# Kernel optimization log

Hardware: AMD Instinct MI355X
Metric: run time of the kernel (lower is better)

## Reference

```python
import jax, jax.numpy as jnp
import numpy as np

N = 50000      # nodes
E = 800000     # edges
XS = 64        # x_size
ES = 32        # edge_attr dim (in_size = XS + ES = 96)
OUT = 64       # out_size
H = 128        # hidden_size
EPS = 1e-5


def _lin_init(k, fan_in, fan_out):
    s = 1.0 / np.sqrt(fan_in)
    kw, kb = jax.random.split(k)
    w = jax.random.uniform(kw, (fan_in, fan_out), minval=-s, maxval=s, dtype=jnp.float32)
    b = jax.random.uniform(kb, (fan_out,), minval=-s, maxval=s, dtype=jnp.float32)
    return w, b


def setup_inputs() -> dict:
    key = jax.random.key(0)
    ks = jax.random.split(key, 12)
    x = jax.random.normal(ks[0], (N, XS), dtype=jnp.float32)
    edge_index = jax.random.randint(ks[1], (2, E), 0, N, dtype=jnp.int64)
    edge_attr = jax.random.normal(ks[2], (E, ES), dtype=jnp.float32)
    u = jax.random.normal(ks[3], (1, 8), dtype=jnp.float32)
    batch = jnp.zeros((N,), dtype=jnp.int64)
    # MLP1: (96->128) LReLU (128->128) LReLU (128->64) LReLU LN(64)
    m1w0, m1b0 = _lin_init(ks[4], XS + ES, H)
    m1w1, m1b1 = _lin_init(ks[5], H, H)
    m1w2, m1b2 = _lin_init(ks[6], H, OUT)
    ln1_g = jnp.ones((OUT,), jnp.float32); ln1_b = jnp.zeros((OUT,), jnp.float32)
    # MLP2: (128->128) LReLU (128->128) LReLU (128->64) LReLU LN(64)
    m2w0, m2b0 = _lin_init(ks[7], XS + OUT, H)
    m2w1, m2b1 = _lin_init(ks[8], H, H)
    m2w2, m2b2 = _lin_init(ks[9], H, OUT)
    ln2_g = jnp.ones((OUT,), jnp.float32); ln2_b = jnp.zeros((OUT,), jnp.float32)
    return dict(x=x, edge_index=edge_index, edge_attr=edge_attr, u=u, batch=batch,
                m1w0=m1w0, m1b0=m1b0, m1w1=m1w1, m1b1=m1b1, m1w2=m1w2, m1b2=m1b2,
                ln1_g=ln1_g, ln1_b=ln1_b,
                m2w0=m2w0, m2b0=m2b0, m2w1=m2w1, m2b1=m2b1, m2w2=m2w2, m2b2=m2b2,
                ln2_g=ln2_g, ln2_b=ln2_b)


def _lrelu(v):
    return jax.nn.leaky_relu(v, 0.01)


def _layernorm(v, g, b):
    mu = jnp.mean(v, axis=-1, keepdims=True)
    var = jnp.mean(jnp.square(v - mu), axis=-1, keepdims=True)
    return (v - mu) * jax.lax.rsqrt(var + EPS) * g + b


def _mlp(h, w0, b0, w1, b1, w2, b2, g, bn):
    h = _lrelu(h @ w0 + b0)
    h = _lrelu(h @ w1 + b1)
    h = _lrelu(h @ w2 + b2)          # activate_last=True
    return _layernorm(h, g, bn)      # layer_norm=True


def reference(x, edge_index, edge_attr, u, batch,
              m1w0, m1b0, m1w1, m1b1, m1w2, m1b2, ln1_g, ln1_b,
              m2w0, m2b0, m2w1, m2b1, m2w2, m2b2, ln2_g, ln2_b):
    row, col = edge_index[0], edge_index[1]
    # gather source nodes, concat edge features -> per-edge MLP
    h = jnp.concatenate([x[row], edge_attr], axis=1)            # [E, 96]
    h = _mlp(h, m1w0, m1b0, m1w1, m1b1, m1w2, m1b2, ln1_g, ln1_b)  # [E, 64]
    # scatter_mean over destination nodes
    agg = jax.ops.segment_sum(h, col, num_segments=N)           # [N, 64]
    cnt = jax.ops.segment_sum(jnp.ones((E,), h.dtype), col, num_segments=N)
    agg = agg / jnp.maximum(cnt, 1.0)[:, None]
    # node update MLP
    h2 = jnp.concatenate([x, agg], axis=1)                      # [N, 128]
    return _mlp(h2, m2w0, m2b0, m2w1, m2b1, m2w2, m2b2, ln2_g, ln2_b)
```

## Files before the change

kernel.cpp:

```cpp
#include <hip/hip_runtime.h>


#define NNODES 50000
#define NEDGES 800000

typedef __bf16 bf16;
typedef __bf16 __attribute__((ext_vector_type(4))) bf16x4;
typedef __bf16 __attribute__((ext_vector_type(8))) bf16x8;
typedef float __attribute__((ext_vector_type(4))) f32x4;

__device__ __forceinline__ f32x4 mfma_bf16(bf16x8 a, bf16x8 b, f32x4 c) {
    return __builtin_amdgcn_mfma_f32_16x16x32_bf16(a, b, c, 0, 0, 0);
}


__global__ void prep_weights(const float* __restrict__ w10, const float* __restrict__ w11,
                             const float* __restrict__ w12, const float* __restrict__ w20,
                             const float* __restrict__ w21, const float* __restrict__ w22,
                             bf16* __restrict__ img) {
    int idx = blockIdx.x * 256 + threadIdx.x;
    float f;
    if (idx < 13312) {
        int n = idx / 104, k = idx % 104;
        f = (k < 96) ? w10[k * 128 + n] : 0.0f;
    } else if (idx < 30720) {
        int t = idx - 13312; int n = t / 136, k = t % 136;
        f = (k < 128) ? w11[k * 128 + n] : 0.0f;
    } else if (idx < 39424) {
        int t = idx - 30720; int n = t / 136, k = t % 136;
        f = (k < 128) ? w12[k * 64 + n] : 0.0f;
    } else if (idx < 56832) {
        int t = idx - 39424; int n = t / 136, k = t % 136;
        f = (k < 128) ? w20[k * 128 + n] : 0.0f;
    } else if (idx < 74240) {
        int t = idx - 56832; int n = t / 136, k = t % 136;
        f = (k < 128) ? w21[k * 128 + n] : 0.0f;
    } else if (idx < 82944) {
        int t = idx - 74240; int n = t / 136, k = t % 136;
        f = (k < 128) ? w22[k * 64 + n] : 0.0f;
    } else {
        return;
    }
    img[idx] = (bf16)f;
}

__global__ __launch_bounds__(256) void edge_mlp(
    const float* __restrict__ x, const int* __restrict__ eidx,
    const float* __restrict__ eattr, const bf16* __restrict__ wimg,
    const float* __restrict__ b0g, const float* __restrict__ b1g,
    const float* __restrict__ b2g, const float* __restrict__ lng,
    const float* __restrict__ lnb, float* __restrict__ agg, float* __restrict__ cnt) {
    __shared__ __align__(16) bf16 wall[39424];
    __shared__ __align__(16) bf16 atile[128 * 104];
    __shared__ __align__(16) bf16 hid[128 * 136];
    __shared__ float bs[448];

    const int tid = threadIdx.x;
    {
        const uint4* src = (const uint4*)wimg;
        uint4* dst = (uint4*)wall;
        for (int i = tid; i < 4928; i += 256) dst[i] = src[i];
    }
    if (tid < 128) { bs[tid] = b0g[tid]; bs[128 + tid] = b1g[tid]; }
    else {
        int t = tid - 128;
        if (t < 64) { bs[256 + t] = b2g[t]; bs[320 + t] = lng[t]; bs[384 + t] = lnb[t]; }
    }
    __syncthreads();

    const int lane = tid & 63;
    const int wv = tid >> 6;
    const int col16 = lane & 15;
    const int quad = lane >> 4;

    float b0r[8], b1r[8], b2r[4], gr[4], br[4];
#pragma unroll
    for (int i = 0; i < 8; i++) { b0r[i] = bs[i * 16 + col16]; b1r[i] = bs[128 + i * 16 + col16]; }
#pragma unroll
    for (int i = 0; i < 4; i++) {
        b2r[i] = bs[256 + i * 16 + col16];
        gr[i] = bs[320 + i * 16 + col16];
        br[i] = bs[384 + i * 16 + col16];
    }

    const bf16* w0t = wall;
    const bf16* w1t = wall + 13312;
    const bf16* w2t = wall + 30720;

    const int ebase = blockIdx.x * 128;
    const f32x4 vzero = {0.0f, 0.0f, 0.0f, 0.0f};

    {
        const int el = tid >> 1, half = tid & 1;
        const int e = ebase + el;
        const int r = eidx[e];
        const float4* xs = (const float4*)(x + (size_t)r * 64);
        bf16* arow = atile + el * 104;
#pragma unroll
        for (int j = 0; j < 8; j++) {
            float4 v = xs[half * 8 + j];
            bf16x4 u = {(bf16)v.x, (bf16)v.y, (bf16)v.z, (bf16)v.w};
            *(bf16x4*)(arow + half * 32 + j * 4) = u;
        }
        const float4* es = (const float4*)(eattr + (size_t)e * 32);
#pragma unroll
        for (int j = 0; j < 4; j++) {
            float4 v = es[half * 4 + j];
            bf16x4 u = {(bf16)v.x, (bf16)v.y, (bf16)v.z, (bf16)v.w};
            *(bf16x4*)(arow + 64 + half * 16 + j * 4) = u;
        }
    }

    const int r0 = wv * 32 + col16;
    const int rw = wv * 32 + quad * 4;

    f32x4 acc1[2][8];
#pragma unroll
    for (int mt = 0; mt < 2; mt++)
#pragma unroll
        for (int nt = 0; nt < 8; nt++) acc1[mt][nt] = vzero;
#pragma unroll
    for (int ks = 0; ks < 3; ks++) {
        bf16x8 a0 = *(const bf16x8*)(atile + r0 * 104 + ks * 32 + quad * 8);
        bf16x8 a1 = *(const bf16x8*)(atile + (r0 + 16) * 104 + ks * 32 + quad * 8);
#pragma unroll
        for (int nt = 0; nt < 8; nt++) {
            bf16x8 b = *(const bf16x8*)(w0t + (nt * 16 + col16) * 104 + ks * 32 + quad * 8);
            acc1[0][nt] = mfma_bf16(a0, b, acc1[0][nt]);
            acc1[1][nt] = mfma_bf16(a1, b, acc1[1][nt]);
        }
    }
#pragma unroll
    for (int mt = 0; mt < 2; mt++)
#pragma unroll
        for (int nt = 0; nt < 8; nt++)
#pragma unroll
            for (int rg = 0; rg < 4; rg++) {
                float v = acc1[mt][nt][rg] + b0r[nt];
                v = (v > 0.0f) ? v : 0.01f * v;
                hid[(rw + mt * 16 + rg) * 136 + nt * 16 + col16] = (bf16)v;
            }

    bf16x8 a2[2][4];
#pragma unroll
    for (int mt = 0; mt < 2; mt++)
#pragma unroll
        for (int ks = 0; ks < 4; ks++)
            a2[mt][ks] = *(const bf16x8*)(hid + (r0 + mt * 16) * 136 + ks * 32 + quad * 8);
    f32x4 acc2[2][8];
#pragma unroll
    for (int mt = 0; mt < 2; mt++)
#pragma unroll
        for (int nt = 0; nt < 8; nt++) acc2[mt][nt] = vzero;
#pragma unroll
    for (int ks = 0; ks < 4; ks++) {
#pragma unroll
        for (int nt = 0; nt < 8; nt++) {
            bf16x8 b = *(const bf16x8*)(w1t + (nt * 16 + col16) * 136 + ks * 32 + quad * 8);
            acc2[0][nt] = mfma_bf16(a2[0][ks], b, acc2[0][nt]);
            acc2[1][nt] = mfma_bf16(a2[1][ks], b, acc2[1][nt]);
        }
    }
#pragma unroll
    for (int mt = 0; mt < 2; mt++)
#pragma unroll
        for (int nt = 0; nt < 8; nt++)
#pragma unroll
            for (int rg = 0; rg < 4; rg++) {
                float v = acc2[mt][nt][rg] + b1r[nt];
                v = (v > 0.0f) ? v : 0.01f * v;
                hid[(rw + mt * 16 + rg) * 136 + nt * 16 + col16] = (bf16)v;
            }

    bf16x8 a3[2][4];
#pragma unroll
    for (int mt = 0; mt < 2; mt++)
#pragma unroll
        for (int ks = 0; ks < 4; ks++)
            a3[mt][ks] = *(const bf16x8*)(hid + (r0 + mt * 16) * 136 + ks * 32 + quad * 8);
    f32x4 acc3[2][4];
#pragma unroll
    for (int mt = 0; mt < 2; mt++)
#pragma unroll
        for (int nt = 0; nt < 4; nt++) acc3[mt][nt] = vzero;
#pragma unroll
    for (int ks = 0; ks < 4; ks++) {
#pragma unroll
        for (int nt = 0; nt < 4; nt++) {
            bf16x8 b = *(const bf16x8*)(w2t + (nt * 16 + col16) * 136 + ks * 32 + quad * 8);
            acc3[0][nt] = mfma_bf16(a3[0][ks], b, acc3[0][nt]);
            acc3[1][nt] = mfma_bf16(a3[1][ks], b, acc3[1][nt]);
        }
    }

    const int* cidx = eidx + NEDGES;
#pragma unroll
    for (int mt = 0; mt < 2; mt++) {
        float vals[4][4];
        float s1[4] = {0.f, 0.f, 0.f, 0.f}, s2[4] = {0.f, 0.f, 0.f, 0.f};
#pragma unroll
        for (int nt = 0; nt < 4; nt++)
#pragma unroll
            for (int rg = 0; rg < 4; rg++) {
                float v = acc3[mt][nt][rg] + b2r[nt];
                v = (v > 0.0f) ? v : 0.01f * v;
                vals[nt][rg] = v;
                s1[rg] += v;
                s2[rg] += v * v;
            }
#pragma unroll
        for (int off = 1; off < 16; off <<= 1) {
#pragma unroll
            for (int rg = 0; rg < 4; rg++) {
                s1[rg] += __shfl_xor(s1[rg], off);
                s2[rg] += __shfl_xor(s2[rg], off);
            }
        }
#pragma unroll
        for (int rg = 0; rg < 4; rg++) {
            float mu = s1[rg] * 0.015625f;
            float var = s2[rg] * 0.015625f - mu * mu;
            float rstd = rsqrtf(var + 1e-5f);
            int e = ebase + rw + mt * 16 + rg;
            int c = cidx[e];
            float* dst = agg + (size_t)c * 64;
#pragma unroll
            for (int nt = 0; nt < 4; nt++) {
                float o = (vals[nt][rg] - mu) * rstd * gr[nt] + br[nt];
                atomicAdd(dst + nt * 16 + col16, o);
            }
            if (col16 == 0) atomicAdd(cnt + c, 1.0f);
        }
    }
}

__global__ __launch_bounds__(256) void node_mlp(
    const float* __restrict__ x, const float* __restrict__ agg,
    const float* __restrict__ cnt, const bf16* __restrict__ wimg,
    const float* __restrict__ b0g, const float* __restrict__ b1g,
    const float* __restrict__ b2g, const float* __restrict__ lng,
    const float* __restrict__ lnb, float* __restrict__ out) {
    __shared__ __align__(16) bf16 wall[43520];
    __shared__ __align__(16) bf16 atile[128 * 136];
    __shared__ __align__(16) bf16 hid[128 * 136];
    __shared__ float bs[448];

    const int tid = threadIdx.x;
    {
        const uint4* src = (const uint4*)wimg;
        uint4* dst = (uint4*)wall;
        for (int i = tid; i < 5440; i += 256) dst[i] = src[i];
    }
    if (tid < 128) { bs[tid] = b0g[tid]; bs[128 + tid] = b1g[tid]; }
    else {
        int t = tid - 128;
        if (t < 64) { bs[256 + t] = b2g[t]; bs[320 + t] = lng[t]; bs[384 + t] = lnb[t]; }
    }
    __syncthreads();

    const int lane = tid & 63;
    const int wv = tid >> 6;
    const int col16 = lane & 15;
    const int quad = lane >> 4;

    float b0r[8], b1r[8], b2r[4], gr[4], br[4];
#pragma unroll
    for (int i = 0; i < 8; i++) { b0r[i] = bs[i * 16 + col16]; b1r[i] = bs[128 + i * 16 + col16]; }
#pragma unroll
    for (int i = 0; i < 4; i++) {
        b2r[i] = bs[256 + i * 16 + col16];
        gr[i] = bs[320 + i * 16 + col16];
        br[i] = bs[384 + i * 16 + col16];
    }

    const bf16* w0t = wall;
    const bf16* w1t = wall + 17408;
    const bf16* w2t = wall + 34816;

    const int nbase = blockIdx.x * 128;
    const f32x4 vzero = {0.0f, 0.0f, 0.0f, 0.0f};

    {
        const int el = tid >> 1, half = tid & 1;
        int i = nbase + el;
        if (i >= NNODES) i = NNODES - 1;
        const float4* xs = (const float4*)(x + (size_t)i * 64);
        bf16* arow = atile + el * 136;
#pragma unroll
        for (int j = 0; j < 8; j++) {
            float4 v = xs[half * 8 + j];
            bf16x4 u = {(bf16)v.x, (bf16)v.y, (bf16)v.z, (bf16)v.w};
            *(bf16x4*)(arow + half * 32 + j * 4) = u;
        }
        float inv = 1.0f / fmaxf(cnt[i], 1.0f);
        const float4* as = (const float4*)(agg + (size_t)i * 64);
#pragma unroll
        for (int j = 0; j < 8; j++) {
            float4 v = as[half * 8 + j];
            bf16x4 u = {(bf16)(v.x * inv), (bf16)(v.y * inv), (bf16)(v.z * inv), (bf16)(v.w * inv)};
            *(bf16x4*)(arow + 64 + half * 32 + j * 4) = u;
        }
    }

    const int r0 = wv * 32 + col16;
    const int rw = wv * 32 + quad * 4;

    f32x4 acc1[2][8];
#pragma unroll
    for (int mt = 0; mt < 2; mt++)
#pragma unroll
        for (int nt = 0; nt < 8; nt++) acc1[mt][nt] = vzero;
#pragma unroll
    for (int ks = 0; ks < 4; ks++) {
        bf16x8 a0 = *(const bf16x8*)(atile + r0 * 136 + ks * 32 + quad * 8);
        bf16x8 a1 = *(const bf16x8*)(atile + (r0 + 16) * 136 + ks * 32 + quad * 8);
#pragma unroll
        for (int nt = 0; nt < 8; nt++) {
            bf16x8 b = *(const bf16x8*)(w0t + (nt * 16 + col16) * 136 + ks * 32 + quad * 8);
            acc1[0][nt] = mfma_bf16(a0, b, acc1[0][nt]);
            acc1[1][nt] = mfma_bf16(a1, b, acc1[1][nt]);
        }
    }
#pragma unroll
    for (int mt = 0; mt < 2; mt++)
#pragma unroll
        for (int nt = 0; nt < 8; nt++)
#pragma unroll
            for (int rg = 0; rg < 4; rg++) {
                float v = acc1[mt][nt][rg] + b0r[nt];
                v = (v > 0.0f) ? v : 0.01f * v;
                hid[(rw + mt * 16 + rg) * 136 + nt * 16 + col16] = (bf16)v;
            }

    bf16x8 a2[2][4];
#pragma unroll
    for (int mt = 0; mt < 2; mt++)
#pragma unroll
        for (int ks = 0; ks < 4; ks++)
            a2[mt][ks] = *(const bf16x8*)(hid + (r0 + mt * 16) * 136 + ks * 32 + quad * 8);
    f32x4 acc2[2][8];
#pragma unroll
    for (int mt = 0; mt < 2; mt++)
#pragma unroll
        for (int nt = 0; nt < 8; nt++) acc2[mt][nt] = vzero;
#pragma unroll
    for (int ks = 0; ks < 4; ks++) {
#pragma unroll
        for (int nt = 0; nt < 8; nt++) {
            bf16x8 b = *(const bf16x8*)(w1t + (nt * 16 + col16) * 136 + ks * 32 + quad * 8);
            acc2[0][nt] = mfma_bf16(a2[0][ks], b, acc2[0][nt]);
            acc2[1][nt] = mfma_bf16(a2[1][ks], b, acc2[1][nt]);
        }
    }
#pragma unroll
    for (int mt = 0; mt < 2; mt++)
#pragma unroll
        for (int nt = 0; nt < 8; nt++)
#pragma unroll
            for (int rg = 0; rg < 4; rg++) {
                float v = acc2[mt][nt][rg] + b1r[nt];
                v = (v > 0.0f) ? v : 0.01f * v;
                hid[(rw + mt * 16 + rg) * 136 + nt * 16 + col16] = (bf16)v;
            }

    bf16x8 a3[2][4];
#pragma unroll
    for (int mt = 0; mt < 2; mt++)
#pragma unroll
        for (int ks = 0; ks < 4; ks++)
            a3[mt][ks] = *(const bf16x8*)(hid + (r0 + mt * 16) * 136 + ks * 32 + quad * 8);
    f32x4 acc3[2][4];
#pragma unroll
    for (int mt = 0; mt < 2; mt++)
#pragma unroll
        for (int nt = 0; nt < 4; nt++) acc3[mt][nt] = vzero;
#pragma unroll
    for (int ks = 0; ks < 4; ks++) {
#pragma unroll
        for (int nt = 0; nt < 4; nt++) {
            bf16x8 b = *(const bf16x8*)(w2t + (nt * 16 + col16) * 136 + ks * 32 + quad * 8);
            acc3[0][nt] = mfma_bf16(a3[0][ks], b, acc3[0][nt]);
            acc3[1][nt] = mfma_bf16(a3[1][ks], b, acc3[1][nt]);
        }
    }

#pragma unroll
    for (int mt = 0; mt < 2; mt++) {
        float vals[4][4];
        float s1[4] = {0.f, 0.f, 0.f, 0.f}, s2[4] = {0.f, 0.f, 0.f, 0.f};
#pragma unroll
        for (int nt = 0; nt < 4; nt++)
#pragma unroll
            for (int rg = 0; rg < 4; rg++) {
                float v = acc3[mt][nt][rg] + b2r[nt];
                v = (v > 0.0f) ? v : 0.01f * v;
                vals[nt][rg] = v;
                s1[rg] += v;
                s2[rg] += v * v;
            }
#pragma unroll
        for (int off = 1; off < 16; off <<= 1) {
#pragma unroll
            for (int rg = 0; rg < 4; rg++) {
                s1[rg] += __shfl_xor(s1[rg], off);
                s2[rg] += __shfl_xor(s2[rg], off);
            }
        }
#pragma unroll
        for (int rg = 0; rg < 4; rg++) {
            float mu = s1[rg] * 0.015625f;
            float var = s2[rg] * 0.015625f - mu * mu;
            float rstd = rsqrtf(var + 1e-5f);
            int i = nbase + rw + mt * 16 + rg;
            if (i < NNODES) {
#pragma unroll
                for (int nt = 0; nt < 4; nt++) {
                    float o = (vals[nt][rg] - mu) * rstd * gr[nt] + br[nt];
                    out[(size_t)i * 64 + nt * 16 + col16] = o;
                }
            }
        }
    }
}

extern "C" void kernel_launch(void* const* d_in, const int* in_sizes, int n_in,
                              void* d_out, int out_size, void* d_ws, size_t ws_size,
                              hipStream_t stream) {
    (void)in_sizes; (void)n_in; (void)out_size; (void)ws_size;
    const float* x     = (const float*)d_in[0];
    const int*   eidx  = (const int*)d_in[1];
    const float* eattr = (const float*)d_in[2];
    const float* m1w0 = (const float*)d_in[5];
    const float* m1b0 = (const float*)d_in[6];
    const float* m1w1 = (const float*)d_in[7];
    const float* m1b1 = (const float*)d_in[8];
    const float* m1w2 = (const float*)d_in[9];
    const float* m1b2 = (const float*)d_in[10];
    const float* ln1g = (const float*)d_in[11];
    const float* ln1b = (const float*)d_in[12];
    const float* m2w0 = (const float*)d_in[13];
    const float* m2b0 = (const float*)d_in[14];
    const float* m2w1 = (const float*)d_in[15];
    const float* m2b1 = (const float*)d_in[16];
    const float* m2w2 = (const float*)d_in[17];
    const float* m2b2 = (const float*)d_in[18];
    const float* ln2g = (const float*)d_in[19];
    const float* ln2b = (const float*)d_in[20];

    char* ws = (char*)d_ws;
    float* agg = (float*)ws;
    float* cnt = (float*)(ws + (size_t)NNODES * 64 * 4);
    bf16* wimg = (bf16*)(ws + (size_t)NNODES * 64 * 4 + NNODES * 4);

    hipMemsetAsync(d_ws, 0, (size_t)NNODES * 65 * 4, stream);
    prep_weights<<<324, 256, 0, stream>>>(m1w0, m1w1, m1w2, m2w0, m2w1, m2w2, wimg);
    edge_mlp<<<NEDGES / 128, 256, 0, stream>>>(x, eidx, eattr, wimg, m1b0, m1b1, m1b2,
                                               ln1g, ln1b, agg, cnt);
    node_mlp<<<(NNODES + 127) / 128, 256, 0, stream>>>(x, agg, cnt, wimg + 39424,
                                                       m2b0, m2b1, m2b2, ln2g, ln2b,
                                                       (float*)d_out);
}
```

Measured before the change: 569.0 us.

## Sort edges by destination and make edge/node MLP kernels persistent

Adds a counting sort of edges by destination node: a histogram, a three-kernel prefix scan, and a scatter that builds a permutation plus packed src/dst indices. The edge MLP then walks the sorted order and merges consecutive rows that share a destination before issuing float atomics. This cuts atomic traffic and contention, and the histogram replaces the per-edge count atomics. Both MLP kernels become persistent grid-stride loops, so the LDS weight image is loaded once per block rather than once per tile. In exchange it adds several small launches and the sort passes, makes the edge_attr reads go through the permutation, and packs the source index into 16 bits, which relies on the node count fitting in that range.

Result: faster. 532.8 us (-6.4%).

```diff
diff --git a/kernel.cpp b/kernel.cpp
--- a/kernel.cpp
+++ b/kernel.cpp
@@ -3,6 +3,8 @@
 
 #define NNODES 50000
 #define NEDGES 800000
+#define NTILES_E 6250
+#define NTILES_N 391
 
 typedef __bf16 bf16;
 typedef __bf16 __attribute__((ext_vector_type(4))) bf16x4;
@@ -12,7 +14,6 @@
 __device__ __forceinline__ f32x4 mfma_bf16(bf16x8 a, bf16x8 b, f32x4 c) {
     return __builtin_amdgcn_mfma_f32_16x16x32_bf16(a, b, c, 0, 0, 0);
 }
-
 
 __global__ void prep_weights(const float* __restrict__ w10, const float* __restrict__ w11,
                              const float* __restrict__ w12, const float* __restrict__ w20,
@@ -44,16 +45,71 @@
     img[idx] = (bf16)f;
 }
 
+__global__ void hist_kernel(const int* __restrict__ col, int* __restrict__ hist) {
+    int i = blockIdx.x * 512 + threadIdx.x;
+    if (i < NEDGES) atomicAdd(hist + col[i], 1);
+}
+
+__global__ void scanA(const int* __restrict__ hist, int* __restrict__ off,
+                      int* __restrict__ csum) {
+    __shared__ int sd[512];
+    int t = threadIdx.x, i = blockIdx.x * 512 + t;
+    int v = (i < NNODES) ? hist[i] : 0;
+    sd[t] = v;
+    __syncthreads();
+    for (int o2 = 1; o2 < 512; o2 <<= 1) {
+        int x = (t >= o2) ? sd[t - o2] : 0;
+        __syncthreads();
+        sd[t] += x;
+        __syncthreads();
+    }
+    if (i < NNODES) off[i] = sd[t] - v;
+    if (t == 511) csum[blockIdx.x] = sd[511];
+}
+
+__global__ void scanB(int* __restrict__ csum) {
+    __shared__ int sd[128];
+    int t = threadIdx.x;
+    int v = (t < 98) ? csum[t] : 0;
+    sd[t] = v;
+    __syncthreads();
+    for (int o2 = 1; o2 < 128; o2 <<= 1) {
+        int x = (t >= o2) ? sd[t - o2] : 0;
+        __syncthreads();
+        sd[t] += x;
+        __syncthreads();
+    }
+    if (t < 98) csum[t] = sd[t] - v;
+}
+
+__global__ void scanC(int* __restrict__ off, const int* __restrict__ csum) {
+    int i = blockIdx.x * 512 + threadIdx.x;
+    if (i < NNODES) off[i] += csum[blockIdx.x];
+}
+
+__global__ void scatter_kernel(const int* __restrict__ eidx, int* __restrict__ off,
+                               int* __restrict__ perm, int* __restrict__ rdS) {
+    int i = blockIdx.x * 512 + threadIdx.x;
+    if (i < NEDGES) {
+        int r = eidx[i], d = eidx[NEDGES + i];
+        int pos = atomicAdd(off + d, 1);
+        perm[pos] = i;
+        rdS[pos] = r | (d << 16);
+    }
+}
+
 __global__ __launch_bounds__(256) void edge_mlp(
-    const float* __restrict__ x, const int* __restrict__ eidx,
-    const float* __restrict__ eattr, const bf16* __restrict__ wimg,
+    const float* __restrict__ x, const int* __restrict__ perm,
+    const int* __restrict__ rdS, const float* __restrict__ eattr,
+    const bf16* __restrict__ wimg,
     const float* __restrict__ b0g, const float* __restrict__ b1g,
     const float* __restrict__ b2g, const float* __restrict__ lng,
-    const float* __restrict__ lnb, float* __restrict__ agg, float* __restrict__ cnt) {
+    const float* __restrict__ lnb, float* __restrict__ agg) {
     __shared__ __align__(16) bf16 wall[39424];
     __shared__ __align__(16) bf16 atile[128 * 104];
     __shared__ __align__(16) bf16 hid[128 * 136];
     __shared__ float bs[448];
+    __shared__ int dstile[128];
 
     const int tid = threadIdx.x;
     {
@@ -87,156 +143,173 @@
     const bf16* w1t = wall + 13312;
     const bf16* w2t = wall + 30720;
 
-    const int ebase = blockIdx.x * 128;
     const f32x4 vzero = {0.0f, 0.0f, 0.0f, 0.0f};
-
-    {
-        const int el = tid >> 1, half = tid & 1;
-        const int e = ebase + el;
-        const int r = eidx[e];
-        const float4* xs = (const float4*)(x + (size_t)r * 64);
-        bf16* arow = atile + el * 104;
-#pragma unroll
-        for (int j = 0; j < 8; j++) {
-            float4 v = xs[half * 8 + j];
-            bf16x4 u = {(bf16)v.x, (bf16)v.y, (bf16)v.z, (bf16)v.w};
-            *(bf16x4*)(arow + half * 32 + j * 4) = u;
-        }
-        const float4* es = (const float4*)(eattr + (size_t)e * 32);
-#pragma unroll
-        for (int j = 0; j < 4; j++) {
-            float4 v = es[half * 4 + j];
-            bf16x4 u = {(bf16)v.x, (bf16)v.y, (bf16)v.z, (bf16)v.w};
-            *(bf16x4*)(arow + 64 + half * 16 + j * 4) = u;
-        }
-    }
-
     const int r0 = wv * 32 + col16;
     const int rw = wv * 32 + quad * 4;
-
-    f32x4 acc1[2][8];
-#pragma unroll
-    for (int mt = 0; mt < 2; mt++)
-#pragma unroll
-        for (int nt = 0; nt < 8; nt++) acc1[mt][nt] = vzero;
-#pragma unroll
-    for (int ks = 0; ks < 3; ks++) {
-        bf16x8 a0 = *(const bf16x8*)(atile + r0 * 104 + ks * 32 + quad * 8);
-        bf16x8 a1 = *(const bf16x8*)(atile + (r0 + 16) * 104 + ks * 32 + quad * 8);
-#pragma unroll
-        for (int nt = 0; nt < 8; nt++) {
-            bf16x8 b = *(const bf16x8*)(w0t + (nt * 16 + col16) * 104 + ks * 32 + quad * 8);
-            acc1[0][nt] = mfma_bf16(a0, b, acc1[0][nt]);
-            acc1[1][nt] = mfma_bf16(a1, b, acc1[1][nt]);
-        }
-    }
-#pragma unroll
-    for (int mt = 0; mt < 2; mt++)
-#pragma unroll
-        for (int nt = 0; nt < 8; nt++)
+    const int el = tid >> 1, half = tid & 1;
+
+    for (int tile = blockIdx.x; tile < NTILES_E; tile += gridDim.x) {
+        const int sbase = tile * 128;
+        {
+            const int s = sbase + el;
+            const int v = rdS[s];
+            const int e = perm[s];
+            const int r = v & 0xFFFF;
+            if (half == 0) dstile[el] = ((unsigned)v) >> 16;
+            const float4* xs = (const float4*)(x + (size_t)r * 64);
+            bf16* arow = atile + el * 104;
+#pragma unroll
+            for (int j = 0; j < 8; j++) {
+                float4 vv = xs[half * 8 + j];
+                bf16x4 u = {(bf16)vv.x, (bf16)vv.y, (bf16)vv.z, (bf16)vv.w};
+                *(bf16x4*)(arow + half * 32 + j * 4) = u;
+            }
+            const float4* es = (const float4*)(eattr + (size_t)e * 32);
+#pragma unroll
+            for (int j = 0; j < 4; j++) {
+                float4 vv = es[half * 4 + j];
+                bf16x4 u = {(bf16)vv.x, (bf16)vv.y, (bf16)vv.z, (bf16)vv.w};
+                *(bf16x4*)(arow + 64 + half * 16 + j * 4) = u;
+            }
+        }
+
+        f32x4 acc1[2][8];
+#pragma unroll
+        for (int mt = 0; mt < 2; mt++)
+#pragma unroll
+            for (int nt = 0; nt < 8; nt++) acc1[mt][nt] = vzero;
+#pragma unroll
+        for (int ks = 0; ks < 3; ks++) {
+            bf16x8 a0 = *(const bf16x8*)(atile + r0 * 104 + ks * 32 + quad * 8);
+            bf16x8 a1 = *(const bf16x8*)(atile + (r0 + 16) * 104 + ks * 32 + quad * 8);
+#pragma unroll
+            for (int nt = 0; nt < 8; nt++) {
+                bf16x8 b = *(const bf16x8*)(w0t + (nt * 16 + col16) * 104 + ks * 32 + quad * 8);
+                acc1[0][nt] = mfma_bf16(a0, b, acc1[0][nt]);
+                acc1[1][nt] = mfma_bf16(a1, b, acc1[1][nt]);
+            }
+        }
+#pragma unroll
+        for (int mt = 0; mt < 2; mt++)
+#pragma unroll
+            for (int nt = 0; nt < 8; nt++)
+#pragma unroll
+                for (int rg = 0; rg < 4; rg++) {
+                    float v = acc1[mt][nt][rg] + b0r[nt];
+                    v = (v > 0.0f) ? v : 0.01f * v;
+                    hid[(rw + mt * 16 + rg) * 136 + nt * 16 + col16] = (bf16)v;
+                }
+
+        bf16x8 a2[2][4];
+#pragma unroll
+        for (int mt = 0; mt < 2; mt++)
+#pragma unroll
+            for (int ks = 0; ks < 4; ks++)
+                a2[mt][ks] = *(const bf16x8*)(hid + (r0 + mt * 16) * 136 + ks * 32 + quad * 8);
+        f32x4 acc2[2][8];
+#pragma unroll
+        for (int mt = 0; mt < 2; mt++)
+#pragma unroll
+            for (int nt = 0; nt < 8; nt++) acc2[mt][nt] = vzero;
+#pragma unroll
+        for (int ks = 0; ks < 4; ks++) {
+#pragma unroll
+            for (int nt = 0; nt < 8; nt++) {
+                bf16x8 b = *(const bf16x8*)(w1t + (nt * 16 + col16) * 136 + ks * 32 + quad * 8);
+                acc2[0][nt] = mfma_bf16(a2[0][ks], b, acc2[0][nt]);
+                acc2[1][nt] = mfma_bf16(a2[1][ks], b, acc2[1][nt]);
+            }
+        }
+#pragma unroll
+        for (int mt = 0; mt < 2; mt++)
+#pragma unroll
+            for (int nt = 0; nt < 8; nt++)
+#pragma unroll
+                for (int rg = 0; rg < 4; rg++) {
+                    float v = acc2[mt][nt][rg] + b1r[nt];
+                    v = (v > 0.0f) ? v : 0.01f * v;
+                    hid[(rw + mt * 16 + rg) * 136 + nt * 16 + col16] = (bf16)v;
+                }
+
+        bf16x8 a3[2][4];
+#pragma unroll
+        for (int mt = 0; mt < 2; mt++)
+#pragma unroll
+            for (int ks = 0; ks < 4; ks++)
+                a3[mt][ks] = *(const bf16x8*)(hid + (r0 + mt * 16) * 136 + ks * 32 + quad * 8);
+        f32x4 acc3[2][4];
+#pragma unroll
+        for (int mt = 0; mt < 2; mt++)
+#pragma unroll
+            for (int nt = 0; nt < 4; nt++) acc3[mt][nt] = vzero;
+#pragma unroll
+        for (int ks = 0; ks < 4; ks++) {
+#pragma unroll
+            for (int nt = 0; nt < 4; nt++) {
+                bf16x8 b = *(const bf16x8*)(w2t + (nt * 16 + col16) * 136 + ks * 32 + quad * 8);
+                acc3[0][nt] = mfma_bf16(a3[0][ks], b, acc3[0][nt]);
+                acc3[1][nt] = mfma_bf16(a3[1][ks], b, acc3[1][nt]);
+            }
+        }
+
+#pragma unroll
+        for (int mt = 0; mt < 2; mt++) {
+            float vals[4][4];
+            float s1[4] = {0.f, 0.f, 0.f, 0.f}, s2[4] = {0.f, 0.f, 0.f, 0.f};
+#pragma unroll
+            for (int nt = 0; nt < 4; nt++)
+#pragma unroll
+                for (int rg = 0; rg < 4; rg++) {
+                    float v = acc3[mt][nt][rg] + b2r[nt];
+                    v = (v > 0.0f) ? v : 0.01f * v;
+                    vals[nt][rg] = v;
+                    s1[rg] += v;
+                    s2[rg] += v * v;
+                }
+#pragma unroll
+            for (int off2 = 1; off2 < 16; off2 <<= 1) {
+#pragma unroll
+                for (int rg = 0; rg < 4; rg++) {
+                    s1[rg] += __shfl_xor(s1[rg], off2);
+                    s2[rg] += __shfl_xor(s2[rg], off2);
+                }
+            }
+            float o[4][4];
+            int dr[4];
 #pragma unroll
             for (int rg = 0; rg < 4; rg++) {
-                float v = acc1[mt][nt][rg] + b0r[nt];
-                v = (v > 0.0f) ? v : 0.01f * v;
-                hid[(rw + mt * 16 + rg) * 136 + nt * 16 + col16] = (bf16)v;
-            }
-
-    bf16x8 a2[2][4];
-#pragma unroll
-    for (int mt = 0; mt < 2; mt++)
-#pragma unroll
-        for (int ks = 0; ks < 4; ks++)
-            a2[mt][ks] = *(const bf16x8*)(hid + (r0 + mt * 16) * 136 + ks * 32 + quad * 8);
-    f32x4 acc2[2][8];
-#pragma unroll
-    for (int mt = 0; mt < 2; mt++)
-#pragma unroll
-        for (int nt = 0; nt < 8; nt++) acc2[mt][nt] = vzero;
-#pragma unroll
-    for (int ks = 0; ks < 4; ks++) {
-#pragma unroll
-        for (int nt = 0; nt < 8; nt++) {
-            bf16x8 b = *(const bf16x8*)(w1t + (nt * 16 + col16) * 136 + ks * 32 + quad * 8);
-            acc2[0][nt] = mfma_bf16(a2[0][ks], b, acc2[0][nt]);
-            acc2[1][nt] = mfma_bf16(a2[1][ks], b, acc2[1][nt]);
-        }
-    }
-#pragma unroll
-    for (int mt = 0; mt < 2; mt++)
-#pragma unroll
-        for (int nt = 0; nt < 8; nt++)
-#pragma unroll
-            for (int rg = 0; rg < 4; rg++) {
-                float v = acc2[mt][nt][rg] + b1r[nt];
-                v = (v > 0.0f) ? v : 0.01f * v;
-                hid[(rw + mt * 16 + rg) * 136 + nt * 16 + col16] = (bf16)v;
-            }
-
-    bf16x8 a3[2][4];
-#pragma unroll
-    for (int mt = 0; mt < 2; mt++)
-#pragma unroll
-        for (int ks = 0; ks < 4; ks++)
-            a3[mt][ks] = *(const bf16x8*)(hid + (r0 + mt * 16) * 136 + ks * 32 + quad * 8);
-    f32x4 acc3[2][4];
-#pragma unroll
-    for (int mt = 0; mt < 2; mt++)
-#pragma unroll
-        for (int nt = 0; nt < 4; nt++) acc3[mt][nt] = vzero;
-#pragma unroll
-    for (int ks = 0; ks < 4; ks++) {
-#pragma unroll
-        for (int nt = 0; nt < 4; nt++) {
-            bf16x8 b = *(const bf16x8*)(w2t + (nt * 16 + col16) * 136 + ks * 32 + quad * 8);
-            acc3[0][nt] = mfma_bf16(a3[0][ks], b, acc3[0][nt]);
-            acc3[1][nt] = mfma_bf16(a3[1][ks], b, acc3[1][nt]);
-        }
-    }
-
-    const int* cidx = eidx + NEDGES;
-#pragma unroll
-    for (int mt = 0; mt < 2; mt++) {
-        float vals[4][4];
-        float s1[4] = {0.f, 0.f, 0.f, 0.f}, s2[4] = {0.f, 0.f, 0.f, 0.f};
-#pragma unroll
-        for (int nt = 0; nt < 4; nt++)
-#pragma unroll
-            for (int rg = 0; rg < 4; rg++) {
-                float v = acc3[mt][nt][rg] + b2r[nt];
-                v = (v > 0.0f) ? v : 0.01f * v;
-                vals[nt][rg] = v;
-                s1[rg] += v;
-                s2[rg] += v * v;
-            }
-#pragma unroll
-        for (int off = 1; off < 16; off <<= 1) {
-#pragma unroll
-            for (int rg = 0; rg < 4; rg++) {
-                s1[rg] += __shfl_xor(s1[rg], off);
-                s2[rg] += __shfl_xor(s2[rg], off);
-            }
-        }
-#pragma unroll
-        for (int rg = 0; rg < 4; rg++) {
-            float mu = s1[rg] * 0.015625f;
-            float var = s2[rg] * 0.015625f - mu * mu;
-            float rstd = rsqrtf(var + 1e-5f);
-            int e = ebase + rw + mt * 16 + rg;
-            int c = cidx[e];
-            float* dst = agg + (size_t)c * 64;
-#pragma unroll
-            for (int nt = 0; nt < 4; nt++) {
-                float o = (vals[nt][rg] - mu) * rstd * gr[nt] + br[nt];
-                atomicAdd(dst + nt * 16 + col16, o);
-            }
-            if (col16 == 0) atomicAdd(cnt + c, 1.0f);
+                float mu = s1[rg] * 0.015625f;
+                float var = s2[rg] * 0.015625f - mu * mu;
+                float rstd = rsqrtf(var + 1e-5f);
+                dr[rg] = dstile[rw + mt * 16 + rg];
+#pragma unroll
+                for (int nt = 0; nt < 4; nt++)
+                    o[nt][rg] = (vals[nt][rg] - mu) * rstd * gr[nt] + br[nt];
+            }
+            float run0 = o[0][0], run1 = o[1][0], run2 = o[2][0], run3 = o[3][0];
+            int cur = dr[0];
+#pragma unroll
+            for (int rg = 1; rg < 4; rg++) {
+                if (dr[rg] != cur) {
+                    float* dst = agg + (size_t)cur * 64 + col16;
+                    atomicAdd(dst, run0); atomicAdd(dst + 16, run1);
+                    atomicAdd(dst + 32, run2); atomicAdd(dst + 48, run3);
+                    run0 = o[0][rg]; run1 = o[1][rg]; run2 = o[2][rg]; run3 = o[3][rg];
+                    cur = dr[rg];
+                } else {
+                    run0 += o[0][rg]; run1 += o[1][rg]; run2 += o[2][rg]; run3 += o[3][rg];
+                }
+            }
+            float* dst = agg + (size_t)cur * 64 + col16;
+            atomicAdd(dst, run0); atomicAdd(dst + 16, run1);
+            atomicAdd(dst + 32, run2); atomicAdd(dst + 48, run3);
         }
     }
 }
 
 __global__ __launch_bounds__(256) void node_mlp(
     const float* __restrict__ x, const float* __restrict__ agg,
-    const float* __restrict__ cnt, const bf16* __restrict__ wimg,
+    const int* __restrict__ hist, const bf16* __restrict__ wimg,
     const float* __restrict__ b0g, const float* __restrict__ b1g,
     const float* __restrict__ b2g, const float* __restrict__ lng,
     const float* __restrict__ lnb, float* __restrict__ out) {
@@ -277,146 +350,148 @@
     const bf16* w1t = wall + 17408;
     const bf16* w2t = wall + 34816;
 
-    const int nbase = blockIdx.x * 128;
     const f32x4 vzero = {0.0f, 0.0f, 0.0f, 0.0f};
-
-    {
-        const int el = tid >> 1, half = tid & 1;
-        int i = nbase + el;
-        if (i >= NNODES) i = NNODES - 1;
-        const float4* xs = (const float4*)(x + (size_t)i * 64);
-        bf16* arow = atile + el * 136;
-#pragma unroll
-        for (int j = 0; j < 8; j++) {
-            float4 v = xs[half * 8 + j];
-            bf16x4 u = {(bf16)v.x, (bf16)v.y, (bf16)v.z, (bf16)v.w};
-            *(bf16x4*)(arow + half * 32 + j * 4) = u;
-        }
-        float inv = 1.0f / fmaxf(cnt[i], 1.0f);
-        const float4* as = (const float4*)(agg + (size_t)i * 64);
-#pragma unroll
-        for (int j = 0; j < 8; j++) {
-            float4 v = as[half * 8 + j];
-            bf16x4 u = {(bf16)(v.x * inv), (bf16)(v.y * inv), (bf16)(v.z * inv), (bf16)(v.w * inv)};
-            *(bf16x4*)(arow + 64 + half * 32 + j * 4) = u;
-        }
-    }
-
     const int r0 = wv * 32 + col16;
     const int rw = wv * 32 + quad * 4;
-
-    f32x4 acc1[2][8];
-#pragma unroll
-    for (int mt = 0; mt < 2; mt++)
-#pragma unroll
-        for (int nt = 0; nt < 8; nt++) acc1[mt][nt] = vzero;
-#pragma unroll
-    for (int ks = 0; ks < 4; ks++) {
-        bf16x8 a0 = *(const bf16x8*)(atile + r0 * 136 + ks * 32 + quad * 8);
-        bf16x8 a1 = *(const bf16x8*)(atile + (r0 + 16) * 136 + ks * 32 + quad * 8);
-#pragma unroll
-        for (int nt = 0; nt < 8; nt++) {
-            bf16x8 b = *(const bf16x8*)(w0t + (nt * 16 + col16) * 136 + ks * 32 + quad * 8);
-            acc1[0][nt] = mfma_bf16(a0, b, acc1[0][nt]);
-            acc1[1][nt] = mfma_bf16(a1, b, acc1[1][nt]);
-        }
-    }
-#pragma unroll
-    for (int mt = 0; mt < 2; mt++)
-#pragma unroll
-        for (int nt = 0; nt < 8; nt++)
+    const int el = tid >> 1, half = tid & 1;
+
+    for (int tile = blockIdx.x; tile < NTILES_N; tile += gridDim.x) {
+        const int nbase = tile * 128;
+        {
+            int i = nbase + el;
+            if (i >= NNODES) i = NNODES - 1;
+            const float4* xs = (const float4*)(x + (size_t)i * 64);
+            bf16* arow = atile + el * 136;
+#pragma unroll
+            for (int j = 0; j < 8; j++) {
+                float4 v = xs[half * 8 + j];
+                bf16x4 u = {(bf16)v.x, (bf16)v.y, (bf16)v.z, (bf16)v.w};
+                *(bf16x4*)(arow + half * 32 + j * 4) = u;
+            }
+            int c = hist[i];
+            float inv = 1.0f / (float)(c > 1 ? c : 1);
+            const float4* as = (const float4*)(agg + (size_t)i * 64);
+#pragma unroll
+            for (int j = 0; j < 8; j++) {
+                float4 v = as[half * 8 + j];
+                bf16x4 u = {(bf16)(v.x * inv), (bf16)(v.y * inv), (bf16)(v.z * inv), (bf16)(v.w * inv)};
+                *(bf16x4*)(arow + 64 + half * 32 + j * 4) = u;
+            }
+        }
+
+        f32x4 acc1[2][8];
+#pragma unroll
+        for (int mt = 0; mt < 2; mt++)
+#pragma unroll
+            for (int nt = 0; nt < 8; nt++) acc1[mt][nt] = vzero;
+#pragma unroll
+        for (int ks = 0; ks < 4; ks++) {
+            bf16x8 a0 = *(const bf16x8*)(atile + r0 * 136 + ks * 32 + quad * 8);
+            bf16x8 a1 = *(const bf16x8*)(atile + (r0 + 16) * 136 + ks * 32 + quad * 8);
+#pragma unroll
+            for (int nt = 0; nt < 8; nt++) {
+                bf16x8 b = *(const bf16x8*)(w0t + (nt * 16 + col16) * 136 + ks * 32 + quad * 8);
+                acc1[0][nt] = mfma_bf16(a0, b, acc1[0][nt]);
+                acc1[1][nt] = mfma_bf16(a1, b, acc1[1][nt]);
+            }
+        }
+#pragma unroll
+        for (int mt = 0; mt < 2; mt++)
+#pragma unroll
+            for (int nt = 0; nt < 8; nt++)
+#pragma unroll
+                for (int rg = 0; rg < 4; rg++) {
+                    float v = acc1[mt][nt][rg] + b0r[nt];
+                    v = (v > 0.0f) ? v : 0.01f * v;
+                    hid[(rw + mt * 16 + rg) * 136 + nt * 16 + col16] = (bf16)v;
+                }
+
+        bf16x8 a2[2][4];
+#pragma unroll
+        for (int mt = 0; mt < 2; mt++)
+#pragma unroll
+            for (int ks = 0; ks < 4; ks++)
+                a2[mt][ks] = *(const bf16x8*)(hid + (r0 + mt * 16) * 136 + ks * 32 + quad * 8);
+        f32x4 acc2[2][8];
+#pragma unroll
+        for (int mt = 0; mt < 2; mt++)
+#pragma unroll
+            for (int nt = 0; nt < 8; nt++) acc2[mt][nt] = vzero;
+#pragma unroll
+        for (int ks = 0; ks < 4; ks++) {
+#pragma unroll
+            for (int nt = 0; nt < 8; nt++) {
+                bf16x8 b = *(const bf16x8*)(w1t + (nt * 16 + col16) * 136 + ks * 32 + quad * 8);
+                acc2[0][nt] = mfma_bf16(a2[0][ks], b, acc2[0][nt]);
+                acc2[1][nt] = mfma_bf16(a2[1][ks], b, acc2[1][nt]);
+            }
+        }
+#pragma unroll
+        for (int mt = 0; mt < 2; mt++)
+#pragma unroll
+            for (int nt = 0; nt < 8; nt++)
+#pragma unroll
+                for (int rg = 0; rg < 4; rg++) {
+                    float v = acc2[mt][nt][rg] + b1r[nt];
+                    v = (v > 0.0f) ? v : 0.01f * v;
+                    hid[(rw + mt * 16 + rg) * 136 + nt * 16 + col16] = (bf16)v;
+                }
+
+        bf16x8 a3[2][4];
+#pragma unroll
+        for (int mt = 0; mt < 2; mt++)
+#pragma unroll
+            for (int ks = 0; ks < 4; ks++)
+                a3[mt][ks] = *(const bf16x8*)(hid + (r0 + mt * 16) * 136 + ks * 32 + quad * 8);
+        f32x4 acc3[2][4];
+#pragma unroll
+        for (int mt = 0; mt < 2; mt++)
+#pragma unroll
+            for (int nt = 0; nt < 4; nt++) acc3[mt][nt] = vzero;
+#pragma unroll
+        for (int ks = 0; ks < 4; ks++) {
+#pragma unroll
+            for (int nt = 0; nt < 4; nt++) {
+                bf16x8 b = *(const bf16x8*)(w2t + (nt * 16 + col16) * 136 + ks * 32 + quad * 8);
+                acc3[0][nt] = mfma_bf16(a3[0][ks], b, acc3[0][nt]);
+                acc3[1][nt] = mfma_bf16(a3[1][ks], b, acc3[1][nt]);
+            }
+        }
+
+#pragma unroll
+        for (int mt = 0; mt < 2; mt++) {
+            float vals[4][4];
+            float s1[4] = {0.f, 0.f, 0.f, 0.f}, s2[4] = {0.f, 0.f, 0.f, 0.f};
+#pragma unroll
+            for (int nt = 0; nt < 4; nt++)
+#pragma unroll
+                for (int rg = 0; rg < 4; rg++) {
+                    float v = acc3[mt][nt][rg] + b2r[nt];
+                    v = (v > 0.0f) ? v : 0.01f * v;
+                    vals[nt][rg] = v;
+                    s1[rg] += v;
+                    s2[rg] += v * v;
+                }
+#pragma unroll
+            for (int off2 = 1; off2 < 16; off2 <<= 1) {
+#pragma unroll
+                for (int rg = 0; rg < 4; rg++) {
+                    s1[rg] += __shfl_xor(s1[rg], off2);
+                    s2[rg] += __shfl_xor(s2[rg], off2);
+                }
+            }
 #pragma unroll
             for (int rg = 0; rg < 4; rg++) {
-                float v = acc1[mt][nt][rg] + b0r[nt];
-                v = (v > 0.0f) ? v : 0.01f * v;
-                hid[(rw + mt * 16 + rg) * 136 + nt * 16 + col16] = (bf16)v;
-            }
-
-    bf16x8 a2[2][4];
-#pragma unroll
-    for (int mt = 0; mt < 2; mt++)
-#pragma unroll
-        for (int ks = 0; ks < 4; ks++)
-            a2[mt][ks] = *(const bf16x8*)(hid + (r0 + mt * 16) * 136 + ks * 32 + quad * 8);
-    f32x4 acc2[2][8];
-#pragma unroll
-    for (int mt = 0; mt < 2; mt++)
-#pragma unroll
-        for (int nt = 0; nt < 8; nt++) acc2[mt][nt] = vzero;
-#pragma unroll
-    for (int ks = 0; ks < 4; ks++) {
-#pragma unroll
-        for (int nt = 0; nt < 8; nt++) {
-            bf16x8 b = *(const bf16x8*)(w1t + (nt * 16 + col16) * 136 + ks * 32 + quad * 8);
-            acc2[0][nt] = mfma_bf16(a2[0][ks], b, acc2[0][nt]);
-            acc2[1][nt] = mfma_bf16(a2[1][ks], b, acc2[1][nt]);
-        }
-    }
-#pragma unroll
-    for (int mt = 0; mt < 2; mt++)
-#pragma unroll
-        for (int nt = 0; nt < 8; nt++)
-#pragma unroll
-            for (int rg = 0; rg < 4; rg++) {
-                float v = acc2[mt][nt][rg] + b1r[nt];
-                v = (v > 0.0f) ? v : 0.01f * v;
-                hid[(rw + mt * 16 + rg) * 136 + nt * 16 + col16] = (bf16)v;
-            }
-
-    bf16x8 a3[2][4];
-#pragma unroll
-    for (int mt = 0; mt < 2; mt++)
-#pragma unroll
-        for (int ks = 0; ks < 4; ks++)
-            a3[mt][ks] = *(const bf16x8*)(hid + (r0 + mt * 16) * 136 + ks * 32 + quad * 8);
-    f32x4 acc3[2][4];
-#pragma unroll
-    for (int mt = 0; mt < 2; mt++)
-#pragma unroll
-        for (int nt = 0; nt < 4; nt++) acc3[mt][nt] = vzero;
-#pragma unroll
-    for (int ks = 0; ks < 4; ks++) {
-#pragma unroll
-        for (int nt = 0; nt < 4; nt++) {
-            bf16x8 b = *(const bf16x8*)(w2t + (nt * 16 + col16) * 136 + ks * 32 + quad * 8);
-            acc3[0][nt] = mfma_bf16(a3[0][ks], b, acc3[0][nt]);
-            acc3[1][nt] = mfma_bf16(a3[1][ks], b, acc3[1][nt]);
-        }
-    }
-
-#pragma unroll
-    for (int mt = 0; mt < 2; mt++) {
-        float vals[4][4];
-        float s1[4] = {0.f, 0.f, 0.f, 0.f}, s2[4] = {0.f, 0.f, 0.f, 0.f};
-#pragma unroll
-        for (int nt = 0; nt < 4; nt++)
-#pragma unroll
-            for (int rg = 0; rg < 4; rg++) {
-                float v = acc3[mt][nt][rg] + b2r[nt];
-                v = (v > 0.0f) ? v : 0.01f * v;
-                vals[nt][rg] = v;
-                s1[rg] += v;
-                s2[rg] += v * v;
-            }
-#pragma unroll
-        for (int off = 1; off < 16; off <<= 1) {
-#pragma unroll
-            for (int rg = 0; rg < 4; rg++) {
-                s1[rg] += __shfl_xor(s1[rg], off);
-                s2[rg] += __shfl_xor(s2[rg], off);
-            }
-        }
-#pragma unroll
-        for (int rg = 0; rg < 4; rg++) {
-            float mu = s1[rg] * 0.015625f;
-            float var = s2[rg] * 0.015625f - mu * mu;
-            float rstd = rsqrtf(var + 1e-5f);
-            int i = nbase + rw + mt * 16 + rg;
-            if (i < NNODES) {
-#pragma unroll
-                for (int nt = 0; nt < 4; nt++) {
-                    float o = (vals[nt][rg] - mu) * rstd * gr[nt] + br[nt];
-                    out[(size_t)i * 64 + nt * 16 + col16] = o;
+                float mu = s1[rg] * 0.015625f;
+                float var = s2[rg] * 0.015625f - mu * mu;
+                float rstd = rsqrtf(var + 1e-5f);
+                int i = nbase + rw + mt * 16 + rg;
+                if (i < NNODES) {
+#pragma unroll
+                    for (int nt = 0; nt < 4; nt++) {
+                        float o = (vals[nt][rg] - mu) * rstd * gr[nt] + br[nt];
+                        out[(size_t)i * 64 + nt * 16 + col16] = o;
+                    }
                 }
             }
         }
@@ -448,15 +523,23 @@
     const float* ln2b = (const float*)d_in[20];
 
     char* ws = (char*)d_ws;
-    float* agg = (float*)ws;
-    float* cnt = (float*)(ws + (size_t)NNODES * 64 * 4);
-    bf16* wimg = (bf16*)(ws + (size_t)NNODES * 64 * 4 + NNODES * 4);
-
-    hipMemsetAsync(d_ws, 0, (size_t)NNODES * 65 * 4, stream);
+    float* agg  = (float*)ws;
+    int*   hist = (int*)(ws + 12800000);
+    int*   off  = (int*)(ws + 13000000);
+    int*   csum = (int*)(ws + 13200000);
+    int*   perm = (int*)(ws + 13200512);
+    int*   rdS  = (int*)(ws + 16400512);
+    bf16*  wimg = (bf16*)(ws + 19600512);
+
+    hipMemsetAsync(d_ws, 0, 13000000, stream);
     prep_weights<<<324, 256, 0, stream>>>(m1w0, m1w1, m1w2, m2w0, m2w1, m2w2, wimg);
-    edge_mlp<<<NEDGES / 128, 256, 0, stream>>>(x, eidx, eattr, wimg, m1b0, m1b1, m1b2,
-                                               ln1g, ln1b, agg, cnt);
-    node_mlp<<<(NNODES + 127) / 128, 256, 0, stream>>>(x, agg, cnt, wimg + 39424,
-                                                       m2b0, m2b1, m2b2, ln2g, ln2b,
-                                                       (float*)d_out);
-}
+    hist_kernel<<<1563, 512, 0, stream>>>(eidx + NEDGES, hist);
+    scanA<<<98, 512, 0, stream>>>(hist, off, csum);
+    scanB<<<1, 128, 0, stream>>>(csum);
+    scanC<<<98, 512, 0, stream>>>(off, csum);
+    scatter_kernel<<<1563, 512, 0, stream>>>(eidx, off, perm, rdS);
+    edge_mlp<<<512, 256, 0, stream>>>(x, perm, rdS, eattr, wimg, m1b0, m1b1, m1b2,
+                                      ln1g, ln1b, agg);
+    node_mlp<<<196, 256, 0, stream>>>(x, agg, hist, wimg + 39424,
+                                      m2b0, m2b1, m2b2, ln2g, ln2b, (float*)d_out);
+}
```
